# Kernel tuning notes

Hardware: AMD Instinct MI355X
Metric: run time of the kernel (lower is better)

The kernel has to match this reference:

```python
import jax, jax.numpy as jnp
import numpy as np

B, T, D, H, NC = 128, 784, 1, 512, 10


def setup_inputs() -> dict:
    key = jax.random.key(0)
    ks = jax.random.split(key, 8)
    x = jax.random.normal(ks[0], (B, T, D), dtype=jnp.float32)
    # UR-LSTM gate weights: chunks [f, r, u, o] each of size H
    Wx = jax.random.normal(ks[1], (D, 4 * H), dtype=jnp.float32) / np.sqrt(D)
    Wh = jax.random.normal(ks[2], (H, 4 * H), dtype=jnp.float32) / np.sqrt(H)
    b = jnp.zeros((4 * H,), dtype=jnp.float32)
    W1 = jax.random.normal(ks[3], (H * T, 256), dtype=jnp.float32) / np.sqrt(H * T)
    b1 = jnp.zeros((256,), dtype=jnp.float32)
    W2 = jax.random.normal(ks[4], (256, NC), dtype=jnp.float32) / np.sqrt(256)
    b2 = jnp.zeros((NC,), dtype=jnp.float32)
    return {"x": x, "Wx": Wx, "Wh": Wh, "b": b, "W1": W1, "b1": b1, "W2": W2, "b2": b2}


def _ur_lstm(x, Wx, Wh, b):
    # x: [B, T, D] -> h sequence [B, T, H]
    Bb = x.shape[0]
    Hh = Wh.shape[0]
    xz = jnp.einsum('btd,dg->btg', x, Wx) + b  # precompute input projection [B,T,4H]

    def step(carry, xz_t):
        h, c = carry
        z = xz_t + h @ Wh  # [B, 4H]
        f, r, u, o = jnp.split(z, 4, axis=-1)
        f = jax.nn.sigmoid(f)
        r = jax.nn.sigmoid(r)
        # refine gate: g = r*(1-(1-f)^2) + (1-r)*f^2
        g = r * (1.0 - (1.0 - f) ** 2) + (1.0 - r) * f ** 2
        c = g * c + (1.0 - g) * jnp.tanh(u)
        h = jax.nn.sigmoid(o) * jnp.tanh(c)
        return (h, c), h

    h0 = jnp.zeros((Bb, Hh), dtype=x.dtype)
    c0 = jnp.zeros((Bb, Hh), dtype=x.dtype)
    (_, _), hs = jax.lax.scan(step, (h0, c0), jnp.swapaxes(xz, 0, 1))
    return jnp.swapaxes(hs, 0, 1)  # [B, T, H]


def reference(x, Wx, Wh, b, W1, b1, W2, b2):
    hs = _ur_lstm(x, Wx, Wh, b)                # [B, T, H]
    flat = hs.reshape(x.shape[0], -1)          # [B, T*H]
    hidden = jax.nn.relu(flat @ W1 + b1)       # [B, 256]
    out = hidden @ W2 + b2                     # [B, NC]
    return out
```

## Files before the change

kernel.cpp:

```cpp
#include <hip/hip_runtime.h>
#include <hip/hip_bf16.h>
#include <stdint.h>

#define B_  128
#define T_  784
#define H_  512
#define G4  2048
#define NC_ 10

#define GB 8
#define GC 32
#define NWG (GB*GC)

typedef __bf16 bf16x8 __attribute__((ext_vector_type(8)));
typedef float  f32x4  __attribute__((ext_vector_type(4)));
typedef unsigned int       u32;
typedef unsigned long long u64;

static __device__ __forceinline__ float bf2f(unsigned short u){
  union { unsigned int i; float f; } v; v.i = ((unsigned int)u) << 16; return v.f;
}
static __device__ __forceinline__ unsigned short f2bf_rn(float f){
  union { float f; unsigned int i; } v; v.f = f;
  unsigned int x = v.i;
  unsigned int lsb = (x >> 16) & 1u;
  x += 0x7fffu + lsb;
  return (unsigned short)(x >> 16);
}

__global__ void prep_wh(const float* __restrict__ Wh,
                        unsigned short* __restrict__ whT_hi,
                        unsigned short* __restrict__ whT_lo){
  int idx = blockIdx.x * blockDim.x + threadIdx.x;
  int kb  = idx >> 11;
  int g   = idx & 2047;
  int k0  = kb * 8;
  unsigned short hi8[8], lo8[8];
  #pragma unroll
  for (int j = 0; j < 8; ++j){
    float v = Wh[(size_t)(k0 + j) * G4 + g];
    unsigned short hi = f2bf_rn(v);
    hi8[j] = hi;
    lo8[j] = f2bf_rn(v - bf2f(hi));
  }
  *(uint4*)(whT_hi + (size_t)g * H_ + k0) = *(const uint4*)hi8;
  *(uint4*)(whT_lo + (size_t)g * H_ + k0) = *(const uint4*)lo8;
}

__global__ __launch_bounds__(256, 1) void scan_k(
    const float* __restrict__ x, const float* __restrict__ Wx,
    const float* __restrict__ bias,
    const unsigned short* __restrict__ whT_hi,
    const unsigned short* __restrict__ whT_lo,
    u32* __restrict__ hbp,
    unsigned short* __restrict__ hs,
    u32* __restrict__ flags)
{
  const int wg  = blockIdx.x;
  const int bg  = wg & 7;
  const int cg  = wg >> 3;
  const int b0  = bg * 16;
  const int c0  = cg * 16;
  const int tid = threadIdx.x;
  const int wv  = tid >> 6;
  const int lane = tid & 63;
  const int nl  = lane & 15;
  const int kc  = lane >> 4;

  __shared__ float xs[16 * 784];
  __shared__ __align__(16) unsigned short hhi[16 * 512];
  __shared__ __align__(16) unsigned short hlo[16 * 512];
  __shared__ float zbuf[16][16][17];

  for (int i = tid; i < 16 * 784; i += 256) xs[i] = x[(size_t)b0 * 784 + i];

  bf16x8 bhi[4][4], blo[4][4];
  #pragma unroll
  for (int q = 0; q < 4; ++q){
    const int gcol = q * 512 + c0 + nl;
    const unsigned short* ph = whT_hi + (size_t)gcol * H_;
    const unsigned short* pl = whT_lo + (size_t)gcol * H_;
    #pragma unroll
    for (int kkl = 0; kkl < 4; ++kkl){
      int ko = (wv * 4 + kkl) * 32 + kc * 8;
      bhi[q][kkl] = *(const bf16x8*)(ph + ko);
      blo[q][kkl] = *(const bf16x8*)(pl + ko);
    }
  }

  const int r_  = tid >> 4;
  const int cl_ = tid & 15;
  float wx4[4], bb4[4];
  #pragma unroll
  for (int q = 0; q < 4; ++q){
    wx4[q] = Wx[q * 512 + c0 + cl_];
    bb4[q] = bias[q * 512 + c0 + cl_];
  }
  float c_st = 0.f;

  u32* const myflag = flags + (bg * 32 + cg);
  const u32* const grpflags = flags + bg * 32;

  __syncthreads();

  for (int t = 0; t < T_; ++t){
    f32x4 zq[4];
    #pragma unroll
    for (int q = 0; q < 4; ++q) zq[q] = (f32x4){0.f, 0.f, 0.f, 0.f};

    if (t > 0){
      {
        int guard = 0;
        for (;;){
          u32 v = 0xffffffffu;
          if (lane < 32)
            v = __hip_atomic_load(grpflags + lane, __ATOMIC_RELAXED, __HIP_MEMORY_SCOPE_AGENT);
          if (__all(v >= (u32)t)) break;
          if (++guard > (1 << 22)) break;
        }
        asm volatile("" ::: "memory");
      }

      const u64* hb8 = (const u64*)(hbp + (size_t)(t & 1) * B_ * H_);
      u64 vv[16];
      #pragma unroll
      for (int j = 0; j < 16; ++j)
        vv[j] = __hip_atomic_load(hb8 + (size_t)(b0 + j) * 256 + tid,
                                  __ATOMIC_RELAXED, __HIP_MEMORY_SCOPE_AGENT);
      #pragma unroll
      for (int j = 0; j < 16; ++j){
        u32 a = (u32)vv[j], b = (u32)(vv[j] >> 32);
        u32 hip_ = (a >> 16) | (b & 0xffff0000u);
        u32 lop_ = (a & 0xffffu) | (b << 16);
        int off = (4 * tid) ^ ((j & 7) << 4);
        *(u32*)((char*)hhi + j * 1024 + off) = hip_;
        *(u32*)((char*)hlo + j * 1024 + off) = lop_;
      }

      f32x4 ahh[4], ahl[4], alh[4];
      #pragma unroll
      for (int q = 0; q < 4; ++q){ ahh[q] = (f32x4){0,0,0,0}; ahl[q] = (f32x4){0,0,0,0}; alh[q] = (f32x4){0,0,0,0}; }

      const int base = nl * 1024;
      const int swz  = (nl & 7) << 4;
      #pragma unroll
      for (int kkl = 0; kkl < 4; ++kkl){
        int bo = (wv * 4 + kkl) * 64 + kc * 16;
        int ad = base + (bo ^ swz);
        bf16x8 ah = *(const bf16x8*)((const char*)hhi + ad);
        bf16x8 al = *(const bf16x8*)((const char*)hlo + ad);
        #pragma unroll
        for (int q = 0; q < 4; ++q){
          ahh[q] = __builtin_amdgcn_mfma_f32_16x16x32_bf16(ah, bhi[q][kkl], ahh[q], 0, 0, 0);
          ahl[q] = __builtin_amdgcn_mfma_f32_16x16x32_bf16(ah, blo[q][kkl], ahl[q], 0, 0, 0);
          alh[q] = __builtin_amdgcn_mfma_f32_16x16x32_bf16(al, bhi[q][kkl], alh[q], 0, 0, 0);
        }
      }
      #pragma unroll
      for (int q = 0; q < 4; ++q) zq[q] = ahh[q] + (ahl[q] + alh[q]);
    }

    #pragma unroll
    for (int q = 0; q < 4; ++q){
      #pragma unroll
      for (int i = 0; i < 4; ++i) zbuf[wv * 4 + q][kc * 4 + i][nl] = zq[q][i];
    }
    __syncthreads();

    {
      float xv = xs[r_ * 784 + t];
      float zf = zbuf[0][r_][cl_] + zbuf[4][r_][cl_] + zbuf[8][r_][cl_]  + zbuf[12][r_][cl_] + xv * wx4[0] + bb4[0];
      float zr = zbuf[1][r_][cl_] + zbuf[5][r_][cl_] + zbuf[9][r_][cl_]  + zbuf[13][r_][cl_] + xv * wx4[1] + bb4[1];
      float zu = zbuf[2][r_][cl_] + zbuf[6][r_][cl_] + zbuf[10][r_][cl_] + zbuf[14][r_][cl_] + xv * wx4[2] + bb4[2];
      float zo = zbuf[3][r_][cl_] + zbuf[7][r_][cl_] + zbuf[11][r_][cl_] + zbuf[15][r_][cl_] + xv * wx4[3] + bb4[3];
      float f  = 1.f / (1.f + expf(-zf));
      float r  = 1.f / (1.f + expf(-zr));
      float omf = 1.f - f;
      float g  = r * (1.f - omf * omf) + (1.f - r) * (f * f);
      c_st = g * c_st + (1.f - g) * tanhf(zu);
      float h = (1.f / (1.f + expf(-zo))) * tanhf(c_st);
      unsigned short hi = f2bf_rn(h);
      unsigned short lo = f2bf_rn(h - bf2f(hi));
      u32 packed = ((u32)hi << 16) | (u32)lo;
      __hip_atomic_store(hbp + (size_t)((t + 1) & 1) * B_ * H_ +
                               (size_t)(b0 + r_) * H_ + (c0 + cl_),
                         packed, __ATOMIC_RELAXED, __HIP_MEMORY_SCOPE_AGENT);
      hs[((size_t)(b0 + r_) * T_ + t) * H_ + (c0 + cl_)] = hi;
    }

    __syncthreads();
    if (tid == 0)
      __hip_atomic_store(myflag, (u32)(t + 1), __ATOMIC_RELAXED, __HIP_MEMORY_SCOPE_AGENT);
  }
}

__global__ __launch_bounds__(256, 1) void mlp1_k(
    const unsigned short* __restrict__ hs,
    const float* __restrict__ W1,
    float* __restrict__ partialT)
{
  const int cm  = blockIdx.x;
  const int tid = threadIdx.x;
  const int wv  = tid >> 6, lane = tid & 63;
  const int nl  = lane & 15, kc = lane >> 4;
  const int m_base = cm * 1568;

  f32x4 acc[4][8];
  #pragma unroll
  for (int i = 0; i < 4; ++i)
    #pragma unroll
    for (int j = 0; j < 8; ++j) acc[i][j] = (f32x4){0, 0, 0, 0};

  for (int ks = 0; ks < 49; ++ks){
    const int m0 = m_base + ks * 32 + kc * 8;
    bf16x8 bf[8];
    #pragma unroll
    for (int nt = 0; nt < 8; ++nt)
      bf[nt] = *(const bf16x8*)(hs + (size_t)(nt * 16 + nl) * 401408 + m0);

    #pragma unroll
    for (int mt = 0; mt < 4; ++mt){
      const int n = wv * 64 + mt * 16 + nl;
      union { bf16x8 v; unsigned short u[8]; } Ah, Al;
      #pragma unroll
      for (int j = 0; j < 8; ++j){
        float av = W1[(size_t)(m0 + j) * 256 + n];
        unsigned short hi = f2bf_rn(av);
        Ah.u[j] = hi;
        Al.u[j] = f2bf_rn(av - bf2f(hi));
      }
      #pragma unroll
      for (int nt = 0; nt < 8; ++nt){
        acc[mt][nt] = __builtin_amdgcn_mfma_f32_16x16x32_bf16(Ah.v, bf[nt], acc[mt][nt], 0, 0, 0);
        acc[mt][nt] = __builtin_amdgcn_mfma_f32_16x16x32_bf16(Al.v, bf[nt], acc[mt][nt], 0, 0, 0);
      }
    }
  }

  #pragma unroll
  for (int mt = 0; mt < 4; ++mt){
    const int n = wv * 64 + mt * 16 + kc * 4;
    #pragma unroll
    for (int nt = 0; nt < 8; ++nt){
      const int b = nt * 16 + nl;
      #pragma unroll
      for (int i = 0; i < 4; ++i)
        partialT[((size_t)cm * 256 + (n + i)) * 128 + b] = acc[mt][nt][i];
    }
  }
}

__global__ void mlp2_k(const float* __restrict__ partialT,
                       const float* __restrict__ b1,
                       float* __restrict__ hiddenT){
  const int n = blockIdx.x;
  const int b = threadIdx.x;
  float s = 0.f;
  for (int cm = 0; cm < 256; ++cm)
    s += partialT[((size_t)cm * 256 + n) * 128 + b];
  s += b1[n];
  hiddenT[n * 128 + b] = s > 0.f ? s : 0.f;
}

__global__ void mlp3_k(const float* __restrict__ hiddenT,
                       const float* __restrict__ W2,
                       const float* __restrict__ b2,
                       float* __restrict__ out){
  const int tid = threadIdx.x;
  for (int oi = tid; oi < B_ * NC_; oi += 256){
    int b = oi / NC_, j = oi % NC_;
    float s = b2[j];
    for (int n = 0; n < 256; ++n)
      s += hiddenT[n * 128 + b] * W2[n * NC_ + j];
    out[oi] = s;
  }
}

extern "C" void kernel_launch(void* const* d_in, const int* in_sizes, int n_in,
                              void* d_out, int out_size, void* d_ws, size_t ws_size,
                              hipStream_t stream){
  const float* x  = (const float*)d_in[0];
  const float* Wx = (const float*)d_in[1];
  const float* Wh = (const float*)d_in[2];
  const float* b  = (const float*)d_in[3];
  const float* W1 = (const float*)d_in[4];
  const float* b1 = (const float*)d_in[5];
  const float* W2 = (const float*)d_in[6];
  const float* b2 = (const float*)d_in[7];

  char* ws = (char*)d_ws;
  size_t o = 0;
  u32*            flags   = (u32*)(ws + o);            o += 1024;
  unsigned short* whT_hi  = (unsigned short*)(ws + o); o += (size_t)G4 * H_ * 2;
  unsigned short* whT_lo  = (unsigned short*)(ws + o); o += (size_t)G4 * H_ * 2;
  u32*            hbp     = (u32*)(ws + o);            o += (size_t)2 * B_ * H_ * 4;
  unsigned short* hs      = (unsigned short*)(ws + o); o += (size_t)B_ * T_ * H_ * 2;
  float*          partialT= (float*)(ws + o);          o += (size_t)256 * 256 * 128 * 4;
  float*          hiddenT = (float*)(ws + o);          o += (size_t)256 * 128 * 4;

  hipMemsetAsync(flags, 0, 1024, stream);
  hipLaunchKernelGGL(prep_wh, dim3(512), dim3(256), 0, stream, Wh, whT_hi, whT_lo);
  hipLaunchKernelGGL(scan_k,  dim3(NWG), dim3(256), 0, stream,
                     x, Wx, b, whT_hi, whT_lo, hbp, hs, flags);
  hipLaunchKernelGGL(mlp1_k,  dim3(256), dim3(256), 0, stream, hs, W1, partialT);
  hipLaunchKernelGGL(mlp2_k,  dim3(256), dim3(128), 0, stream, partialT, b1, hiddenT);
  hipLaunchKernelGGL(mlp3_k,  dim3(1),   dim3(256), 0, stream, hiddenT, W2, b2, (float*)d_out);
}
```

Measured before the change: 2.458 ms.

## Load recurrent h directly into MFMA registers and use fast sigmoid/tanh

Each lane now reads its MFMA A-operand fragment of the previous hidden state straight from global memory into registers, removing the LDS staging of hi/lo bf16 planes and the associated shared-memory writes and reads on the serial critical path. Sigmoid and tanh switch to hardware reciprocal and fast exp intrinsics. A large unused LDS pad, written only under an impossible blockDim condition, is added, apparently to keep per-CU LDS usage high so only one workgroup fits per CU. The direct loads are less coalesced than before, and the fast math loses some accuracy.

New measurement: 3.013 ms. 22.6% more time.

```diff
diff --git a/kernel.cpp b/kernel.cpp
--- a/kernel.cpp
+++ b/kernel.cpp
@@ -26,6 +26,13 @@
   unsigned int lsb = (x >> 16) & 1u;
   x += 0x7fffu + lsb;
   return (unsigned short)(x >> 16);
+}
+
+static __device__ __forceinline__ float fsig(float z){
+  return __builtin_amdgcn_rcpf(1.f + __expf(-z));
+}
+static __device__ __forceinline__ float ftanh(float z){
+  return 2.f * __builtin_amdgcn_rcpf(1.f + __expf(-2.f * z)) - 1.f;
 }
 
 __global__ void prep_wh(const float* __restrict__ Wh,
@@ -68,9 +75,9 @@
   const int kc  = lane >> 4;
 
   __shared__ float xs[16 * 784];
-  __shared__ __align__(16) unsigned short hhi[16 * 512];
-  __shared__ __align__(16) unsigned short hlo[16 * 512];
   __shared__ float zbuf[16][16][17];
+  __shared__ float ldspad[8192];
+  if ((int)blockDim.y == 7) ldspad[tid] = 1.f;
 
   for (int i = tid; i < 16 * 784; i += 256) xs[i] = x[(size_t)b0 * 784 + i];
 
@@ -121,39 +128,35 @@
         asm volatile("" ::: "memory");
       }
 
-      const u64* hb8 = (const u64*)(hbp + (size_t)(t & 1) * B_ * H_);
+      const u64* rowp = (const u64*)(hbp + (size_t)(t & 1) * B_ * H_) +
+                        (size_t)(b0 + nl) * 256 + (wv * 64 + kc * 4);
       u64 vv[16];
       #pragma unroll
-      for (int j = 0; j < 16; ++j)
-        vv[j] = __hip_atomic_load(hb8 + (size_t)(b0 + j) * 256 + tid,
-                                  __ATOMIC_RELAXED, __HIP_MEMORY_SCOPE_AGENT);
-      #pragma unroll
-      for (int j = 0; j < 16; ++j){
-        u32 a = (u32)vv[j], b = (u32)(vv[j] >> 32);
-        u32 hip_ = (a >> 16) | (b & 0xffff0000u);
-        u32 lop_ = (a & 0xffffu) | (b << 16);
-        int off = (4 * tid) ^ ((j & 7) << 4);
-        *(u32*)((char*)hhi + j * 1024 + off) = hip_;
-        *(u32*)((char*)hlo + j * 1024 + off) = lop_;
-      }
+      for (int kkl = 0; kkl < 4; ++kkl)
+        #pragma unroll
+        for (int jj = 0; jj < 4; ++jj)
+          vv[kkl * 4 + jj] = __hip_atomic_load(rowp + kkl * 16 + jj,
+                                 __ATOMIC_RELAXED, __HIP_MEMORY_SCOPE_AGENT);
 
       f32x4 ahh[4], ahl[4], alh[4];
       #pragma unroll
       for (int q = 0; q < 4; ++q){ ahh[q] = (f32x4){0,0,0,0}; ahl[q] = (f32x4){0,0,0,0}; alh[q] = (f32x4){0,0,0,0}; }
 
-      const int base = nl * 1024;
-      const int swz  = (nl & 7) << 4;
       #pragma unroll
       for (int kkl = 0; kkl < 4; ++kkl){
-        int bo = (wv * 4 + kkl) * 64 + kc * 16;
-        int ad = base + (bo ^ swz);
-        bf16x8 ah = *(const bf16x8*)((const char*)hhi + ad);
-        bf16x8 al = *(const bf16x8*)((const char*)hlo + ad);
+        union { bf16x8 v; u32 w[4]; } ah, al;
+        #pragma unroll
+        for (int jj = 0; jj < 4; ++jj){
+          u32 a = (u32)vv[kkl * 4 + jj];
+          u32 b = (u32)(vv[kkl * 4 + jj] >> 32);
+          ah.w[jj] = (a >> 16) | (b & 0xffff0000u);
+          al.w[jj] = (a & 0xffffu) | (b << 16);
+        }
         #pragma unroll
         for (int q = 0; q < 4; ++q){
-          ahh[q] = __builtin_amdgcn_mfma_f32_16x16x32_bf16(ah, bhi[q][kkl], ahh[q], 0, 0, 0);
-          ahl[q] = __builtin_amdgcn_mfma_f32_16x16x32_bf16(ah, blo[q][kkl], ahl[q], 0, 0, 0);
-          alh[q] = __builtin_amdgcn_mfma_f32_16x16x32_bf16(al, bhi[q][kkl], alh[q], 0, 0, 0);
+          ahh[q] = __builtin_amdgcn_mfma_f32_16x16x32_bf16(ah.v, bhi[q][kkl], ahh[q], 0, 0, 0);
+          ahl[q] = __builtin_amdgcn_mfma_f32_16x16x32_bf16(ah.v, blo[q][kkl], ahl[q], 0, 0, 0);
+          alh[q] = __builtin_amdgcn_mfma_f32_16x16x32_bf16(al.v, bhi[q][kkl], alh[q], 0, 0, 0);
         }
       }
       #pragma unroll
@@ -173,12 +176,12 @@
       float zr = zbuf[1][r_][cl_] + zbuf[5][r_][cl_] + zbuf[9][r_][cl_]  + zbuf[13][r_][cl_] + xv * wx4[1] + bb4[1];
       float zu = zbuf[2][r_][cl_] + zbuf[6][r_][cl_] + zbuf[10][r_][cl_] + zbuf[14][r_][cl_] + xv * wx4[2] + bb4[2];
       float zo = zbuf[3][r_][cl_] + zbuf[7][r_][cl_] + zbuf[11][r_][cl_] + zbuf[15][r_][cl_] + xv * wx4[3] + bb4[3];
-      float f  = 1.f / (1.f + expf(-zf));
-      float r  = 1.f / (1.f + expf(-zr));
+      float f  = fsig(zf);
+      float r  = fsig(zr);
       float omf = 1.f - f;
       float g  = r * (1.f - omf * omf) + (1.f - r) * (f * f);
-      c_st = g * c_st + (1.f - g) * tanhf(zu);
-      float h = (1.f / (1.f + expf(-zo))) * tanhf(c_st);
+      c_st = g * c_st + (1.f - g) * ftanh(zu);
+      float h = fsig(zo) * ftanh(c_st);
       unsigned short hi = f2bf_rn(h);
       unsigned short lo = f2bf_rn(h - bf2f(hi));
       u32 packed = ((u32)hi << 16) | (u32)lo;
```
